# Performance work log

Measured on AMD Instinct MI355X. Metric: run time of the kernel, lower is better.

## Reference

```python
import jax, jax.numpy as jnp
import numpy as np

N_HEADS = 16
HEAD_DIM = 64
ROPE_BASE = 10000.0
EPS = 1e-6


def _rope_tables(T, hd, dtype):
    inv_freq = 1.0 / (ROPE_BASE ** (jnp.arange(0, hd, 2, dtype=jnp.float32) / hd))
    freqs = jnp.arange(T, dtype=jnp.float32)[:, None] * inv_freq[None, :]  # [T, hd/2]
    cos = jnp.cos(freqs)[None, :, None, :].astype(dtype)  # [1,T,1,hd/2]
    sin = jnp.sin(freqs)[None, :, None, :].astype(dtype)
    return cos, sin


def _apply_rope(x, cos, sin):
    d = x.shape[-1] // 2
    x1, x2 = x[..., :d], x[..., d:]
    return jnp.concatenate([x1 * cos + x2 * sin, -x1 * sin + x2 * cos], axis=-1)


def setup_inputs() -> dict:
    key = jax.random.key(0)
    k1, k2, k3, k4 = jax.random.split(key, 4)
    B, T, C = 4, 1024, 1024
    x = jax.random.normal(k1, (B, T, C), dtype=jnp.float32)
    W_qkv = jax.random.normal(k2, (3 * C, C), dtype=jnp.float32) * (1.0 / np.sqrt(C))
    W_out = jax.random.normal(k3, (C, C), dtype=jnp.float32) * (1.0 / np.sqrt(C))
    # learnable per-head curvature, init = exp(randn) * base_curvature (base=1.0)
    hyp_k = jnp.exp(jax.random.normal(k4, (1, N_HEADS, 1, 1), dtype=jnp.float32))
    return {"x": x, "W_qkv": W_qkv, "W_out": W_out, "hyp_k": hyp_k}


def reference(x, W_qkv, W_out, hyp_k):
    B, T, C = x.shape
    H, hd = N_HEADS, HEAD_DIM
    qkv = x @ W_qkv.T  # [B,T,3C]
    q, k, v = jnp.split(qkv, 3, axis=-1)
    q = q.reshape(B, T, H, hd)
    k = k.reshape(B, T, H, hd)
    v = v.reshape(B, T, H, hd)

    cos, sin = _rope_tables(T, hd, x.dtype)
    q = _apply_rope(q, cos, sin)
    k = _apply_rope(k, cos, sin)

    # [B,H,T,hd]
    q = q.transpose(0, 2, 1, 3)
    k = k.transpose(0, 2, 1, 3)
    v = v.transpose(0, 2, 1, 3)

    # Lorentz lift: x0 = sqrt(k + ||x||^2); inner = -x0*y0 + <x,y>;
    # dist = sqrt(k) * arccosh(-inner / k)  (geoopt Lorentz convention)
    kc = hyp_k[:, :, :, 0]  # [1,H,1]
    q0 = jnp.sqrt(kc + jnp.sum(q * q, axis=-1))  # [B,H,T]
    k0 = jnp.sqrt(kc + jnp.sum(k * k, axis=-1))  # [B,H,T]
    inner = jnp.einsum('bhld,bhsd->bhls', q, k) - q0[..., None] * k0[:, :, None, :]
    arg = jnp.maximum(-inner / hyp_k, 1.0 + EPS)
    dis = jnp.sqrt(hyp_k) * jnp.arccosh(arg)  # [B,H,L,S]

    attn_weight = 1.0 / (EPS + dis)
    causal = jnp.tril(jnp.ones((T, T), dtype=bool))
    attn_weight = jnp.where(causal, attn_weight, -jnp.inf)
    attn = jax.nn.softmax(attn_weight, axis=-1)
    out = jnp.einsum('bhls,bhsd->bhld', attn, v)  # [B,H,T,hd]
    out = out.transpose(0, 2, 1, 3).reshape(B, T, C)
    return out @ W_out.T
```

## Files before the change

kernel.cpp:

```cpp
#include <hip/hip_runtime.h>

#define B_ 4
#define T_ 1024
#define C_ 1024
#define H_ 16
#define HD_ 64

typedef short bf16x8 __attribute__((ext_vector_type(8)));
typedef float f32x4 __attribute__((ext_vector_type(4)));

__device__ __forceinline__ ushort f2bf(float f) {
    union { float f; unsigned u; } v; v.f = f;
    unsigned u = v.u;
    unsigned r = (u + 0x7fffu + ((u >> 16) & 1u)) >> 16;
    return (ushort)r;
}

__device__ __forceinline__ f32x4 mfma16(bf16x8 a, bf16x8 b, f32x4 c) {
    return __builtin_amdgcn_mfma_f32_16x16x32_bf16(a, b, c, 0, 0, 0);
}

__device__ __forceinline__ bf16x8 lds_frag(const ushort* base, int row, int byteoff) {
    int addr = (row * 128 + byteoff) ^ ((row & 7) << 4);
    uint4 u = *(const uint4*)((const char*)base + addr);
    return __builtin_bit_cast(bf16x8, u);
}

__device__ __forceinline__ bf16x8 lds_frag_v(const ushort* base, int d, int byteoff) {
    int addr = (d * 128 + byteoff) ^ ((((d & 7) ^ (d >> 3)) & 7) << 4);
    uint4 u = *(const uint4*)((const char*)base + addr);
    return __builtin_bit_cast(bf16x8, u);
}

__device__ __forceinline__ bf16x8 lds_frag_p(const ushort* base, int row, int byteoff) {
    int addr = (row * 128 + byteoff) ^ (((row >> 2) & 3) << 5);
    uint4 u = *(const uint4*)((const char*)base + addr);
    return __builtin_bit_cast(bf16x8, u);
}

__device__ __forceinline__ void stage128(ushort* sbase, const ushort* gtile, int wv, int lane) {
    const int srow = lane >> 3;
    const ushort* g0 = gtile + (size_t)srow * C_ + ((((lane & 7) ^ srow)) << 3);
#pragma unroll
    for (int i = 0; i < 4; ++i) {
        int w = wv * 4 + i;
        const ushort* g = g0 + (size_t)(w * 8) * C_;
        ushort* l = sbase + w * 512;
        __builtin_amdgcn_global_load_lds((const __attribute__((address_space(1))) void*)g,
                                         (__attribute__((address_space(3))) void*)l, 16, 0, 0);
    }
}

__global__ void cast_bf16(const float* __restrict__ in, ushort* __restrict__ out, int n) {
    int i = (blockIdx.x * 256 + threadIdx.x) * 4;
    if (i >= n) return;
    float4 v = *(const float4*)(in + i);
    ushort4 o = make_ushort4(f2bf(v.x), f2bf(v.y), f2bf(v.z), f2bf(v.w));
    *(ushort4*)(out + i) = o;
}

#define GEMM_COMPUTE(As, Bs)                                                              \
    {                                                                                     \
        _Pragma("unroll")                                                                 \
        for (int ks = 0; ks < 2; ++ks) {                                                  \
            bf16x8 af[4], bfr[4];                                                         \
            _Pragma("unroll")                                                             \
            for (int mf = 0; mf < 4; ++mf)                                                \
                af[mf] = lds_frag(As, wr * 64 + mf * 16 + (lane & 15),                    \
                                  ks * 64 + ((lane >> 4) << 4));                          \
            _Pragma("unroll")                                                             \
            for (int nf = 0; nf < 4; ++nf)                                                \
                bfr[nf] = lds_frag(Bs, wc * 64 + nf * 16 + (lane & 15),                   \
                                   ks * 64 + ((lane >> 4) << 4));                         \
            _Pragma("unroll")                                                             \
            for (int mf = 0; mf < 4; ++mf)                                                \
                _Pragma("unroll")                                                         \
                for (int nf = 0; nf < 4; ++nf)                                            \
                    acc[mf][nf] = mfma16(af[mf], bfr[nf], acc[mf][nf]);                   \
        }                                                                                 \
    }

__global__ __launch_bounds__(256) void gemm_qkv(
    const ushort* __restrict__ Xb, const ushort* __restrict__ Wb,
    const float* __restrict__ hyp,
    ushort* __restrict__ Qo, ushort* __restrict__ Ko, ushort* __restrict__ Vo,
    float* __restrict__ q0g, float* __restrict__ k0g)
{
    __shared__ ushort As0[128 * 64], Bs0[128 * 64];
    __shared__ ushort As1[128 * 64], Bs1[128 * 64];
    const int tid = threadIdx.x, lane = tid & 63, wv = tid >> 6;
    const int wr = wv >> 1, wc = wv & 1;
    const int m0 = blockIdx.x * 128, n0 = blockIdx.y * 128;
    const ushort* Asrc = Xb + (size_t)m0 * C_;
    const ushort* Bsrc = Wb + (size_t)n0 * C_;

    f32x4 acc[4][4] = {};

    stage128(As0, Asrc, wv, lane);
    stage128(Bs0, Bsrc, wv, lane);
    __syncthreads();

    for (int kt = 0; kt < 16; kt += 2) {
        if (kt + 1 < 16) {
            stage128(As1, Asrc + (kt + 1) * 64, wv, lane);
            stage128(Bs1, Bsrc + (kt + 1) * 64, wv, lane);
        }
        GEMM_COMPUTE(As0, Bs0);
        __syncthreads();
        if (kt + 2 < 16) {
            stage128(As0, Asrc + (kt + 2) * 64, wv, lane);
            stage128(Bs0, Bsrc + (kt + 2) * 64, wv, lane);
        }
        GEMM_COMPUTE(As1, Bs1);
        __syncthreads();
    }

    const int sector = n0 >> 10;
    const int h = ((n0 & 1023) >> 6) + wc;
    const float kc = hyp[h];
    const float inv_k = 1.0f / kc;
    float invf[2];
    invf[0] = __expf(-0.28782313662425572f * (float)(lane & 15));
    invf[1] = __expf(-0.28782313662425572f * (float)(16 + (lane & 15)));

#pragma unroll
    for (int mf = 0; mf < 4; ++mf) {
        float o[4][4];
#pragma unroll
        for (int nf = 0; nf < 4; ++nf)
#pragma unroll
            for (int r = 0; r < 4; ++r) o[nf][r] = acc[mf][nf][r];

        if (sector < 2) {
#pragma unroll
            for (int p = 0; p < 2; ++p) {
#pragma unroll
                for (int r = 0; r < 4; ++r) {
                    int m = m0 + wr * 64 + mf * 16 + ((lane >> 4) << 2) + r;
                    int t = m & (T_ - 1);
                    float sn, cs; __sincosf((float)t * invf[p], &sn, &cs);
                    float x1 = o[p][r], x2 = o[p + 2][r];
                    o[p][r]     =  x1 * cs + x2 * sn;
                    o[p + 2][r] = -x1 * sn + x2 * cs;
                }
            }
        }

#pragma unroll
        for (int r = 0; r < 4; ++r) {
            int m = m0 + wr * 64 + mf * 16 + ((lane >> 4) << 2) + r;
            int b = m >> 10, t = m & (T_ - 1);
            int bh = b * H_ + h;
            size_t base = ((size_t)bh * T_ + t) * HD_;
            float nrm = 0.f;
#pragma unroll
            for (int nf = 0; nf < 4; ++nf) {
                int d = nf * 16 + (lane & 15);
                float v = o[nf][r];
                nrm += v * v;
                ushort bv = f2bf(sector == 1 ? v * inv_k : v);
                if (sector == 0)      Qo[base + d] = bv;
                else if (sector == 1) Ko[base + d] = bv;
                else                  Vo[base + d] = bv;
            }
            if (sector < 2) {
#pragma unroll
                for (int mk = 1; mk < 16; mk <<= 1) nrm += __shfl_xor(nrm, mk);
                if ((lane & 15) == 0) {
                    float v0 = sqrtf(kc + nrm);
                    if (sector == 0) q0g[(size_t)bh * T_ + t] = v0;
                    else             k0g[(size_t)bh * T_ + t] = v0 * inv_k;
                }
            }
        }
    }
}

__global__ __launch_bounds__(256, 2) void attn_fwd(
    const ushort* __restrict__ Q, const ushort* __restrict__ K, const ushort* __restrict__ V,
    const float* __restrict__ q0g, const float* __restrict__ k0g,
    const float* __restrict__ hyp, ushort* __restrict__ AO)
{
    __shared__ ushort Ks[64 * 64];
    __shared__ ushort Vts[64 * 64];
    __shared__ ushort Ps[8][16 * 64];
    __shared__ float k0s[64];

    const int tid = threadIdx.x, lane = tid & 63, wv = tid >> 6;
    const int pr = blockIdx.x >> 6;
    const int bh = blockIdx.x & 63;
    const int h = bh & (H_ - 1);
    const int qa = pr, qb = 15 - pr, nt = qb + 1;
    const float c3 = sqrtf(hyp[h]) * 0.48045301391820142f;
    const float e3 = 6.931471805599453e-07f;

    const ushort* Kb = K + (size_t)bh * T_ * HD_;
    const ushort* Vb = V + (size_t)bh * T_ * HD_;

    bf16x8 aqA[2], aqB[2];
    {
        const ushort* qA = Q + ((size_t)bh * T_ + qa * 64 + wv * 16 + (lane & 15)) * HD_;
        const ushort* qB = Q + ((size_t)bh * T_ + qb * 64 + wv * 16 + (lane & 15)) * HD_;
#pragma unroll
        for (int ks = 0; ks < 2; ++ks) {
            aqA[ks] = __builtin_bit_cast(bf16x8, *(const uint4*)(qA + ks * 32 + ((lane >> 4) << 3)));
            aqB[ks] = __builtin_bit_cast(bf16x8, *(const uint4*)(qB + ks * 32 + ((lane >> 4) << 3)));
        }
    }
    float q0A[4], q0B[4];
#pragma unroll
    for (int r = 0; r < 4; ++r) {
        int rr = wv * 16 + ((lane >> 4) << 2) + r;
        q0A[r] = q0g[(size_t)bh * T_ + qa * 64 + rr];
        q0B[r] = q0g[(size_t)bh * T_ + qb * 64 + rr];
    }

    f32x4 oaccA[4] = {}, oaccB[4] = {};
    float lpA[4] = {}, lpB[4] = {};

    const int krow = tid >> 3, koff = tid & 7;
    const int sp = tid >> 3, dc = tid & 7;
    uint4 kv0, kv1, vv0, vv1;
    float kz = 0.f;
    auto issue = [&](int s0) {
        kv0 = *(const uint4*)(Kb + (size_t)(s0 + krow) * HD_ + koff * 8);
        kv1 = *(const uint4*)(Kb + (size_t)(s0 + 32 + krow) * HD_ + koff * 8);
        vv0 = *(const uint4*)(Vb + (size_t)(s0 + 2 * sp) * HD_ + dc * 8);
        vv1 = *(const uint4*)(Vb + (size_t)(s0 + 2 * sp + 1) * HD_ + dc * 8);
        if (tid < 64) kz = k0g[(size_t)bh * T_ + s0 + tid];
    };

    auto geom = [&](const f32x4* sc, const float* q0, const float* k0r, float p[4][4]) {
#pragma unroll
        for (int r = 0; r < 4; ++r)
#pragma unroll
            for (int sf = 0; sf < 4; ++sf) {
                float arg = fmaf(q0[r], k0r[sf], -sc[sf][r]);
                arg = fmaxf(arg, 1.0f + 1e-6f);
                float t = fmaf(arg, arg, -1.0f);
                float u = arg + __builtin_amdgcn_sqrtf(t);
                float l2 = __builtin_amdgcn_logf(u);
                float w2 = fmaf(l2, c3, e3);
                float rv = fminf(__builtin_amdgcn_rcpf(w2), 30.0f);
                p[sf][r] = __builtin_amdgcn_exp2f(rv);
            }
    };
    auto mask_diag = [&](float p[4][4]) {
        const int qloc = wv * 16 + ((lane >> 4) << 2);
#pragma unroll
        for (int r = 0; r < 4; ++r)
#pragma unroll
            for (int sf = 0; sf < 4; ++sf)
                if (sf * 16 + (lane & 15) > qloc + r) p[sf][r] = 0.f;
    };
    auto pv_step = [&](float p[4][4], ushort* ps, const bf16x8 (&vf)[2][4],
                       f32x4* oacc, float* lp) {
#pragma unroll
        for (int r = 0; r < 4; ++r) {
            int row = ((lane >> 4) << 2) + r;
#pragma unroll
            for (int sf = 0; sf < 4; ++sf) {
                int addr = (row * 128 + (sf * 16 + (lane & 15)) * 2) ^ (((row >> 2) & 3) << 5);
                *(ushort*)((char*)ps + addr) = f2bf(p[sf][r]);
            }
            lp[r] += (p[0][r] + p[1][r]) + (p[2][r] + p[3][r]);
        }
#pragma unroll
        for (int ks = 0; ks < 2; ++ks) {
            bf16x8 ap = lds_frag_p(ps, lane & 15, ks * 64 + ((lane >> 4) << 4));
#pragma unroll
            for (int df = 0; df < 4; ++df)
                oacc[df] = mfma16(ap, vf[ks][df], oacc[df]);
        }
    };

    issue(0);

    for (int it = 0; it < nt; ++it) {
        const bool actA = (it <= qa);
        __syncthreads();
        {
            *(uint4*)((char*)Ks + ((tid * 16) ^ ((krow & 7) << 4))) = kv0;
            int c1 = tid + 256;
            *(uint4*)((char*)Ks + ((c1 * 16) ^ (((c1 >> 3) & 7) << 4))) = kv1;
            union { uint4 v; ushort u[8]; } a, b;
            a.v = vv0; b.v = vv1;
#pragma unroll
            for (int j = 0; j < 8; ++j) {
                int d = dc * 8 + j;
                uint pack = (uint)a.u[j] | ((uint)b.u[j] << 16);
                *(uint*)((char*)Vts + ((d * 128 + sp * 4) ^ (((j ^ dc) & 7) << 4))) = pack;
            }
            if (tid < 64) k0s[tid] = kz;
        }
        if (it + 1 < nt) issue((it + 1) * 64);
        __syncthreads();

        bf16x8 bk[2][4];
#pragma unroll
        for (int ks = 0; ks < 2; ++ks)
#pragma unroll
            for (int sf = 0; sf < 4; ++sf)
                bk[ks][sf] = lds_frag(Ks, sf * 16 + (lane & 15), ks * 64 + ((lane >> 4) << 4));

        float k0r[4];
#pragma unroll
        for (int sf = 0; sf < 4; ++sf) k0r[sf] = k0s[sf * 16 + (lane & 15)];

        f32x4 scB[4] = {};
#pragma unroll
        for (int ks = 0; ks < 2; ++ks)
#pragma unroll
            for (int sf = 0; sf < 4; ++sf)
                scB[sf] = mfma16(aqB[ks], bk[ks][sf], scB[sf]);
        f32x4 scA[4] = {};
        if (actA) {
#pragma unroll
            for (int ks = 0; ks < 2; ++ks)
#pragma unroll
                for (int sf = 0; sf < 4; ++sf)
                    scA[sf] = mfma16(aqA[ks], bk[ks][sf], scA[sf]);
        }

        bf16x8 vf[2][4];
#pragma unroll
        for (int ks = 0; ks < 2; ++ks)
#pragma unroll
            for (int df = 0; df < 4; ++df)
                vf[ks][df] = lds_frag_v(Vts, df * 16 + (lane & 15), ks * 64 + ((lane >> 4) << 4));

        float pB[4][4];
        geom(scB, q0B, k0r, pB);
        if (it == qb) mask_diag(pB);
        pv_step(pB, Ps[wv * 2 + 1], vf, oaccB, lpB);

        if (actA) {
            float pA[4][4];
            geom(scA, q0A, k0r, pA);
            if (it == qa) mask_diag(pA);
            pv_step(pA, Ps[wv * 2 + 0], vf, oaccA, lpA);
        }
    }

    const int b = bh >> 4;
    auto epi = [&](f32x4* oacc, float* lp, int qt) {
#pragma unroll
        for (int r = 0; r < 4; ++r) {
            float s = lp[r];
#pragma unroll
            for (int mk = 1; mk < 16; mk <<= 1) s += __shfl_xor(s, mk);
            float invl = __builtin_amdgcn_rcpf(s);
            int t = qt * 64 + wv * 16 + ((lane >> 4) << 2) + r;
            size_t base = ((size_t)b * T_ + t) * C_ + h * HD_;
#pragma unroll
            for (int df = 0; df < 4; ++df)
                AO[base + df * 16 + (lane & 15)] = f2bf(oacc[df][r] * invl);
        }
    };
    epi(oaccA, lpA, qa);
    epi(oaccB, lpB, qb);
}

__global__ __launch_bounds__(256) void gemm_out(
    const ushort* __restrict__ Ab, const ushort* __restrict__ Wb, float* __restrict__ Out)
{
    __shared__ ushort As0[128 * 64], Bs0[128 * 64];
    __shared__ ushort As1[128 * 64], Bs1[128 * 64];
    const int tid = threadIdx.x, lane = tid & 63, wv = tid >> 6;
    const int wr = wv >> 1, wc = wv & 1;
    const int m0 = blockIdx.x * 128, n0 = blockIdx.y * 128;
    const ushort* Asrc = Ab + (size_t)m0 * C_;
    const ushort* Bsrc = Wb + (size_t)n0 * C_;

    f32x4 acc[4][4] = {};

    stage128(As0, Asrc, wv, lane);
    stage128(Bs0, Bsrc, wv, lane);
    __syncthreads();

    for (int kt = 0; kt < 16; kt += 2) {
        if (kt + 1 < 16) {
            stage128(As1, Asrc + (kt + 1) * 64, wv, lane);
            stage128(Bs1, Bsrc + (kt + 1) * 64, wv, lane);
        }
        GEMM_COMPUTE(As0, Bs0);
        __syncthreads();
        if (kt + 2 < 16) {
            stage128(As0, Asrc + (kt + 2) * 64, wv, lane);
            stage128(Bs0, Bsrc + (kt + 2) * 64, wv, lane);
        }
        GEMM_COMPUTE(As1, Bs1);
        __syncthreads();
    }

#pragma unroll
    for (int mf = 0; mf < 4; ++mf)
#pragma unroll
        for (int r = 0; r < 4; ++r) {
            int m = m0 + wr * 64 + mf * 16 + ((lane >> 4) << 2) + r;
#pragma unroll
            for (int nf = 0; nf < 4; ++nf) {
                int n = n0 + wc * 64 + nf * 16 + (lane & 15);
                Out[(size_t)m * C_ + n] = acc[mf][nf][r];
            }
        }
}

extern "C" void kernel_launch(void* const* d_in, const int* in_sizes, int n_in,
                              void* d_out, int out_size, void* d_ws, size_t ws_size,
                              hipStream_t stream)
{
    const float* x    = (const float*)d_in[0];
    const float* wqkv = (const float*)d_in[1];
    const float* wout = (const float*)d_in[2];
    const float* hyp  = (const float*)d_in[3];

    char* ws = (char*)d_ws;
    ushort* xb    = (ushort*)(ws + 0);
    ushort* wqkvb = (ushort*)(ws + 8388608);
    ushort* woutb = (ushort*)(ws + 14680064);
    ushort* Qb    = (ushort*)(ws + 16777216);
    ushort* Kb    = (ushort*)(ws + 25165824);
    ushort* Vb    = (ushort*)(ws + 33554432);
    ushort* Ab    = (ushort*)(ws + 41943040);
    float*  q0    = (float*)(ws + 50331648);
    float*  k0    = (float*)(ws + 50593792);

    cast_bf16<<<4096, 256, 0, stream>>>(x, xb, 4194304);
    cast_bf16<<<3072, 256, 0, stream>>>(wqkv, wqkvb, 3145728);
    cast_bf16<<<1024, 256, 0, stream>>>(wout, woutb, 1048576);

    gemm_qkv<<<dim3(32, 24), 256, 0, stream>>>(xb, wqkvb, hyp, Qb, Kb, Vb, q0, k0);
    attn_fwd<<<512, 256, 0, stream>>>(Qb, Kb, Vb, q0, k0, hyp, Ab);
    gemm_out<<<dim3(32, 8), 256, 0, stream>>>(Ab, woutb, (float*)d_out);
}
```

Before: 106.5 us.

## Use 128x64 GEMM tiles with register-staged single-buffer LDS pipeline

Both projection GEMMs drop from 128x128 tiles to 128x64, doubling the grid size. Each wave now owns 32 rows across the full 64 columns. The asynchronous global_load_lds double buffering is replaced by a register prefetch: the next K-tile is loaded into registers, then written into a single swizzled LDS buffer between two barriers. This is meant to raise occupancy and block count, but each block reuses less data from its tile. It also adds an extra barrier per K step and a register round-trip for the staged tiles.

After: 275.0 us. +158.3%, slower.

```diff
diff --git a/kernel.cpp b/kernel.cpp
--- a/kernel.cpp
+++ b/kernel.cpp
@@ -38,16 +38,14 @@
     return __builtin_bit_cast(bf16x8, u);
 }
 
-__device__ __forceinline__ void stage128(ushort* sbase, const ushort* gtile, int wv, int lane) {
-    const int srow = lane >> 3;
-    const ushort* g0 = gtile + (size_t)srow * C_ + ((((lane & 7) ^ srow)) << 3);
-#pragma unroll
-    for (int i = 0; i < 4; ++i) {
-        int w = wv * 4 + i;
-        const ushort* g = g0 + (size_t)(w * 8) * C_;
-        ushort* l = sbase + w * 512;
-        __builtin_amdgcn_global_load_lds((const __attribute__((address_space(1))) void*)g,
-                                         (__attribute__((address_space(3))) void*)l, 16, 0, 0);
+__device__ __forceinline__ void stage_tile(ushort* sdst, const ushort* gsrc, int ld, int tid) {
+#pragma unroll
+    for (int it = 0; it < 2; ++it) {
+        int c = tid + it * 256;
+        int row = c >> 3, off = c & 7;
+        uint4 v = *(const uint4*)(gsrc + (size_t)row * ld + off * 8);
+        int addr = (c * 16) ^ ((row & 7) << 4);
+        *(uint4*)((char*)sdst + addr) = v;
     }
 }
 
@@ -59,21 +57,47 @@
     *(ushort4*)(out + i) = o;
 }
 
-#define GEMM_COMPUTE(As, Bs)                                                              \
+struct GemmState { uint4 a[4]; uint4 b[2]; };
+
+__device__ __forceinline__ void g_issue(GemmState& st, const ushort* Asrc, const ushort* Bsrc,
+                                        int tid) {
+    const int row = tid >> 3, off = (tid & 7) * 8;
+#pragma unroll
+    for (int i = 0; i < 4; ++i)
+        st.a[i] = *(const uint4*)(Asrc + (size_t)(i * 32 + row) * C_ + off);
+#pragma unroll
+    for (int i = 0; i < 2; ++i)
+        st.b[i] = *(const uint4*)(Bsrc + (size_t)(i * 32 + row) * C_ + off);
+}
+
+__device__ __forceinline__ void g_write(const GemmState& st, ushort* As, ushort* Bs, int tid) {
+#pragma unroll
+    for (int i = 0; i < 4; ++i) {
+        int c = tid + i * 256, row = c >> 3;
+        *(uint4*)((char*)As + ((c * 16) ^ ((row & 7) << 4))) = st.a[i];
+    }
+#pragma unroll
+    for (int i = 0; i < 2; ++i) {
+        int c = tid + i * 256, row = c >> 3;
+        *(uint4*)((char*)Bs + ((c * 16) ^ ((row & 7) << 4))) = st.b[i];
+    }
+}
+
+#define GEMM_COMPUTE_128x64(As, Bs)                                                       \
     {                                                                                     \
         _Pragma("unroll")                                                                 \
         for (int ks = 0; ks < 2; ++ks) {                                                  \
-            bf16x8 af[4], bfr[4];                                                         \
+            bf16x8 af[2], bfr[4];                                                         \
             _Pragma("unroll")                                                             \
-            for (int mf = 0; mf < 4; ++mf)                                                \
-                af[mf] = lds_frag(As, wr * 64 + mf * 16 + (lane & 15),                    \
+            for (int mf = 0; mf < 2; ++mf)                                                \
+                af[mf] = lds_frag(As, wv * 32 + mf * 16 + (lane & 15),                    \
                                   ks * 64 + ((lane >> 4) << 4));                          \
             _Pragma("unroll")                                                             \
             for (int nf = 0; nf < 4; ++nf)                                                \
-                bfr[nf] = lds_frag(Bs, wc * 64 + nf * 16 + (lane & 15),                   \
+                bfr[nf] = lds_frag(Bs, nf * 16 + (lane & 15),                             \
                                    ks * 64 + ((lane >> 4) << 4));                         \
             _Pragma("unroll")                                                             \
-            for (int mf = 0; mf < 4; ++mf)                                                \
+            for (int mf = 0; mf < 2; ++mf)                                                \
                 _Pragma("unroll")                                                         \
                 for (int nf = 0; nf < 4; ++nf)                                            \
                     acc[mf][nf] = mfma16(af[mf], bfr[nf], acc[mf][nf]);                   \
@@ -86,37 +110,27 @@
     ushort* __restrict__ Qo, ushort* __restrict__ Ko, ushort* __restrict__ Vo,
     float* __restrict__ q0g, float* __restrict__ k0g)
 {
-    __shared__ ushort As0[128 * 64], Bs0[128 * 64];
-    __shared__ ushort As1[128 * 64], Bs1[128 * 64];
+    __shared__ ushort As[128 * 64];
+    __shared__ ushort Bs[64 * 64];
     const int tid = threadIdx.x, lane = tid & 63, wv = tid >> 6;
-    const int wr = wv >> 1, wc = wv & 1;
-    const int m0 = blockIdx.x * 128, n0 = blockIdx.y * 128;
+    const int m0 = blockIdx.x * 128, n0 = blockIdx.y * 64;
     const ushort* Asrc = Xb + (size_t)m0 * C_;
     const ushort* Bsrc = Wb + (size_t)n0 * C_;
 
-    f32x4 acc[4][4] = {};
-
-    stage128(As0, Asrc, wv, lane);
-    stage128(Bs0, Bsrc, wv, lane);
-    __syncthreads();
-
-    for (int kt = 0; kt < 16; kt += 2) {
-        if (kt + 1 < 16) {
-            stage128(As1, Asrc + (kt + 1) * 64, wv, lane);
-            stage128(Bs1, Bsrc + (kt + 1) * 64, wv, lane);
-        }
-        GEMM_COMPUTE(As0, Bs0);
-        __syncthreads();
-        if (kt + 2 < 16) {
-            stage128(As0, Asrc + (kt + 2) * 64, wv, lane);
-            stage128(Bs0, Bsrc + (kt + 2) * 64, wv, lane);
-        }
-        GEMM_COMPUTE(As1, Bs1);
-        __syncthreads();
+    GemmState st;
+    g_issue(st, Asrc, Bsrc, tid);
+
+    f32x4 acc[2][4] = {};
+    for (int kt = 0; kt < 16; ++kt) {
+        __syncthreads();
+        g_write(st, As, Bs, tid);
+        if (kt + 1 < 16) g_issue(st, Asrc + (kt + 1) * 64, Bsrc + (kt + 1) * 64, tid);
+        __syncthreads();
+        GEMM_COMPUTE_128x64(As, Bs);
     }
 
     const int sector = n0 >> 10;
-    const int h = ((n0 & 1023) >> 6) + wc;
+    const int h = (n0 & 1023) >> 6;
     const float kc = hyp[h];
     const float inv_k = 1.0f / kc;
     float invf[2];
@@ -124,7 +138,7 @@
     invf[1] = __expf(-0.28782313662425572f * (float)(16 + (lane & 15)));
 
 #pragma unroll
-    for (int mf = 0; mf < 4; ++mf) {
+    for (int mf = 0; mf < 2; ++mf) {
         float o[4][4];
 #pragma unroll
         for (int nf = 0; nf < 4; ++nf)
@@ -136,7 +150,7 @@
             for (int p = 0; p < 2; ++p) {
 #pragma unroll
                 for (int r = 0; r < 4; ++r) {
-                    int m = m0 + wr * 64 + mf * 16 + ((lane >> 4) << 2) + r;
+                    int m = m0 + wv * 32 + mf * 16 + ((lane >> 4) << 2) + r;
                     int t = m & (T_ - 1);
                     float sn, cs; __sincosf((float)t * invf[p], &sn, &cs);
                     float x1 = o[p][r], x2 = o[p + 2][r];
@@ -148,7 +162,7 @@
 
 #pragma unroll
         for (int r = 0; r < 4; ++r) {
-            int m = m0 + wr * 64 + mf * 16 + ((lane >> 4) << 2) + r;
+            int m = m0 + wv * 32 + mf * 16 + ((lane >> 4) << 2) + r;
             int b = m >> 10, t = m & (T_ - 1);
             int bh = b * H_ + h;
             size_t base = ((size_t)bh * T_ + t) * HD_;
@@ -364,43 +378,33 @@
 __global__ __launch_bounds__(256) void gemm_out(
     const ushort* __restrict__ Ab, const ushort* __restrict__ Wb, float* __restrict__ Out)
 {
-    __shared__ ushort As0[128 * 64], Bs0[128 * 64];
-    __shared__ ushort As1[128 * 64], Bs1[128 * 64];
+    __shared__ ushort As[128 * 64];
+    __shared__ ushort Bs[64 * 64];
     const int tid = threadIdx.x, lane = tid & 63, wv = tid >> 6;
-    const int wr = wv >> 1, wc = wv & 1;
-    const int m0 = blockIdx.x * 128, n0 = blockIdx.y * 128;
+    const int m0 = blockIdx.x * 128, n0 = blockIdx.y * 64;
     const ushort* Asrc = Ab + (size_t)m0 * C_;
     const ushort* Bsrc = Wb + (size_t)n0 * C_;
 
-    f32x4 acc[4][4] = {};
-
-    stage128(As0, Asrc, wv, lane);
-    stage128(Bs0, Bsrc, wv, lane);
-    __syncthreads();
-
-    for (int kt = 0; kt < 16; kt += 2) {
-        if (kt + 1 < 16) {
-            stage128(As1, Asrc + (kt + 1) * 64, wv, lane);
-            stage128(Bs1, Bsrc + (kt + 1) * 64, wv, lane);
-        }
-        GEMM_COMPUTE(As0, Bs0);
-        __syncthreads();
-        if (kt + 2 < 16) {
-            stage128(As0, Asrc + (kt + 2) * 64, wv, lane);
-            stage128(Bs0, Bsrc + (kt + 2) * 64, wv, lane);
-        }
-        GEMM_COMPUTE(As1, Bs1);
-        __syncthreads();
-    }
-
-#pragma unroll
-    for (int mf = 0; mf < 4; ++mf)
+    GemmState st;
+    g_issue(st, Asrc, Bsrc, tid);
+
+    f32x4 acc[2][4] = {};
+    for (int kt = 0; kt < 16; ++kt) {
+        __syncthreads();
+        g_write(st, As, Bs, tid);
+        if (kt + 1 < 16) g_issue(st, Asrc + (kt + 1) * 64, Bsrc + (kt + 1) * 64, tid);
+        __syncthreads();
+        GEMM_COMPUTE_128x64(As, Bs);
+    }
+
+#pragma unroll
+    for (int mf = 0; mf < 2; ++mf)
 #pragma unroll
         for (int r = 0; r < 4; ++r) {
-            int m = m0 + wr * 64 + mf * 16 + ((lane >> 4) << 2) + r;
+            int m = m0 + wv * 32 + mf * 16 + ((lane >> 4) << 2) + r;
 #pragma unroll
             for (int nf = 0; nf < 4; ++nf) {
-                int n = n0 + wc * 64 + nf * 16 + (lane & 15);
+                int n = n0 + nf * 16 + (lane & 15);
                 Out[(size_t)m * C_ + n] = acc[mf][nf][r];
             }
         }
@@ -430,7 +434,7 @@
     cast_bf16<<<3072, 256, 0, stream>>>(wqkv, wqkvb, 3145728);
     cast_bf16<<<1024, 256, 0, stream>>>(wout, woutb, 1048576);
 
-    gemm_qkv<<<dim3(32, 24), 256, 0, stream>>>(xb, wqkvb, hyp, Qb, Kb, Vb, q0, k0);
+    gemm_qkv<<<dim3(32, 48), 256, 0, stream>>>(xb, wqkvb, hyp, Qb, Kb, Vb, q0, k0);
     attn_fwd<<<512, 256, 0, stream>>>(Qb, Kb, Vb, q0, k0, hyp, Ab);
-    gemm_out<<<dim3(32, 8), 256, 0, stream>>>(Ab, woutb, (float*)d_out);
-}
+    gemm_out<<<dim3(32, 16), 256, 0, stream>>>(Ab, woutb, (float*)d_out);
+}
```
